# Performance work log

Hardware: AMD Instinct MI355X
Metric: run time of the kernel (lower is better)

## Reference

```python
import jax, jax.numpy as jnp
import numpy as np

E = 1024   # embed_dim
H = 1024   # hidden_dim
NH = 16    # num_heads
HD = H // NH
B, P, C = 2, 1024, 1024


def _layernorm(x, g, b):
    m = jnp.mean(x, axis=-1, keepdims=True)
    v = jnp.mean((x - m) ** 2, axis=-1, keepdims=True)
    return (x - m) / jnp.sqrt(v + 1e-5) * g + b


def _attention(problem, context, Wq, bq, Wk, bk, Wv, bv, mask, num_heads, head_dim, head_out_dim):
    # Faithful to source: head axis LAST in the reshape, mask added AFTER softmax.
    batch = problem.shape[0]
    q = (problem @ Wq + bq).reshape(batch, -1, head_dim, num_heads)      # b i d h
    k = (context @ Wk + bk).reshape(batch, -1, head_dim, num_heads)      # b j d h
    v = (context @ Wv + bv).reshape(batch, -1, head_out_dim, num_heads)  # b j o h
    scores = jnp.einsum('bidh,bjdh->bijh', q, k) / jnp.sqrt(jnp.asarray(head_dim, q.dtype))
    p = jax.nn.softmax(scores, axis=2)
    if mask is not None:
        p = p + mask[..., None]
    out = jnp.einsum('bijh,bjoh->bioh', p, v)
    return out.reshape(batch, -1, head_out_dim * num_heads)


def setup_inputs() -> dict:
    key = jax.random.key(0)
    ks = jax.random.split(key, 20)
    s = 0.02
    inp = {
        'x': jax.random.normal(ks[0], (B, P, E), jnp.float32),
        'context': jax.random.normal(ks[1], (B, C, E), jnp.float32),
        'causal_mask': jnp.zeros((B, P, P), jnp.float32),
        'problem_pad_mask': jnp.zeros((B, P, P), jnp.float32),
        'context_pad_mask': jnp.zeros((B, P, C), jnp.float32),
        # self-attn params (out_dim = E)
        'sa_Wq': jax.random.normal(ks[2], (E, H), jnp.float32) * s, 'sa_bq': jnp.zeros((H,), jnp.float32),
        'sa_Wk': jax.random.normal(ks[3], (E, H), jnp.float32) * s, 'sa_bk': jnp.zeros((H,), jnp.float32),
        'sa_Wv': jax.random.normal(ks[4], (E, E), jnp.float32) * s, 'sa_bv': jnp.zeros((E,), jnp.float32),
        # cross-attn params
        'ca_Wq': jax.random.normal(ks[5], (E, H), jnp.float32) * s, 'ca_bq': jnp.zeros((H,), jnp.float32),
        'ca_Wk': jax.random.normal(ks[6], (E, H), jnp.float32) * s, 'ca_bk': jnp.zeros((H,), jnp.float32),
        'ca_Wv': jax.random.normal(ks[7], (E, E), jnp.float32) * s, 'ca_bv': jnp.zeros((E,), jnp.float32),
        # layernorms
        'ln1_g': jnp.ones((E,), jnp.float32), 'ln1_b': jnp.zeros((E,), jnp.float32),
        'ln2_g': jnp.ones((E,), jnp.float32), 'ln2_b': jnp.zeros((E,), jnp.float32),
        'ln3_g': jnp.ones((E,), jnp.float32), 'ln3_b': jnp.zeros((E,), jnp.float32),
        # mlp
        'mlp_W1': jax.random.normal(ks[8], (E, H), jnp.float32) * s, 'mlp_b1': jnp.zeros((H,), jnp.float32),
        'mlp_W2': jax.random.normal(ks[9], (H, E), jnp.float32) * s, 'mlp_b2': jnp.zeros((E,), jnp.float32),
    }
    return inp


def reference(x, context, causal_mask, problem_pad_mask, context_pad_mask,
              sa_Wq, sa_bq, sa_Wk, sa_bk, sa_Wv, sa_bv,
              ca_Wq, ca_bq, ca_Wk, ca_bk, ca_Wv, ca_bv,
              ln1_g, ln1_b, ln2_g, ln2_b, ln3_g, ln3_b,
              mlp_W1, mlp_b1, mlp_W2, mlp_b2):
    self_attn_mask = causal_mask + problem_pad_mask
    xc = x
    x = _attention(x, x, sa_Wq, sa_bq, sa_Wk, sa_bk, sa_Wv, sa_bv, self_attn_mask, NH, HD, E // NH)
    x = _layernorm(x, ln1_g, ln1_b) + xc
    xc = x
    x = _attention(x, context, ca_Wq, ca_bq, ca_Wk, ca_bk, ca_Wv, ca_bv, context_pad_mask, NH, HD, E // NH)
    x = _layernorm(x, ln2_g, ln2_b) + xc
    xc = x
    x = jax.nn.relu(x @ mlp_W1 + mlp_b1) @ mlp_W2 + mlp_b2
    return _layernorm(x, ln3_g, ln3_b) + xc
```

## Files before the change

kernel.cpp:

```cpp
#include <hip/hip_runtime.h>
#include <math.h>

#define NHEADS 16

typedef __attribute__((ext_vector_type(8))) short bf16x8;
typedef __attribute__((ext_vector_type(4))) float f32x4;

__device__ inline short f2b(float f) {
  unsigned u = __float_as_uint(f);
  u += 0x7fffu + ((u >> 16) & 1u);
  return (short)(u >> 16);
}
__device__ inline float b2f(short s) {
  return __uint_as_float(((unsigned)(unsigned short)s) << 16);
}
__device__ inline void gld16(const void* g, void* l) {
  __builtin_amdgcn_global_load_lds(
      (const __attribute__((address_space(1))) unsigned int*)g,
      (__attribute__((address_space(3))) unsigned int*)l, 16, 0, 0);
}
#define MFMA16(a, b, c) __builtin_amdgcn_mfma_f32_16x16x32_bf16(a, b, c, 0, 0, 0)

__global__ __launch_bounds__(256) void prep_all(
    const float* __restrict__ x, const float* __restrict__ ctx,
    const float* __restrict__ cm, const float* __restrict__ ppm,
    const float* __restrict__ cpm,
    const float* sabq, const float* sabk, const float* sabv,
    const float* cabk, const float* cabv, const float* cabq,
    short* __restrict__ XB, short* __restrict__ CTXB,
    short* __restrict__ MBSA, short* __restrict__ MBCA,
    float* __restrict__ qkvb, float* __restrict__ kvb,
    float* __restrict__ qpb, unsigned* __restrict__ kmaxu) {
  const int blk = blockIdx.x;
  const int t = threadIdx.x;
  const int n4 = 2048 * 1024 / 4;
  if (blk < 8192) {
    int seg = blk >> 11;
    int i = (blk & 2047) * 256 + t;
    if (i >= n4) return;
    float4 va;
    short* out;
    if (seg == 0) { va = ((const float4*)x)[i]; out = XB; }
    else if (seg == 1) { va = ((const float4*)ctx)[i]; out = CTXB; }
    else if (seg == 2) {
      va = ((const float4*)cm)[i];
      float4 vb = ((const float4*)ppm)[i];
      va.x += vb.x; va.y += vb.y; va.z += vb.z; va.w += vb.w;
      out = MBSA;
    } else { va = ((const float4*)cpm)[i]; out = MBCA; }
    short4 s;
    s.x = f2b(va.x); s.y = f2b(va.y); s.z = f2b(va.z); s.w = f2b(va.w);
    ((short4*)out)[i] = s;
  } else {
    if (blk == 8192 && t < 64) kmaxu[t] = 0u;
    int i = (blk - 8192) * 256 + t;
    if (i >= 6144) return;
    int j = i & 1023;
    int pj = ((j & 63) << 4) | (j >> 6);
    int sec = i >> 10;
    if (sec == 0) qkvb[j] = sabq[pj];
    else if (sec == 1) qkvb[1024 + j] = sabk[pj];
    else if (sec == 2) qkvb[2048 + j] = sabv[pj];
    else if (sec == 3) kvb[j] = cabk[pj];
    else if (sec == 4) kvb[1024 + j] = cabv[pj];
    else qpb[j] = cabq[pj];
  }
}

__global__ __launch_bounds__(256) void wtrans(
    const float* W0, const float* W1, const float* W2, const float* W3,
    const float* W4, const float* W5, const float* W6, const float* W7,
    short* __restrict__ out) {
  __shared__ float t[64][65];
  const float* W;
  switch (blockIdx.z) {
    case 0: W = W0; break; case 1: W = W1; break;
    case 2: W = W2; break; case 3: W = W3; break;
    case 4: W = W4; break; case 5: W = W5; break;
    case 6: W = W6; break; default: W = W7; break;
  }
  const int permute = (blockIdx.z < 6) ? 1 : 0;
  short* o = out + (size_t)blockIdx.z * 1024 * 1024;
  const int tid = threadIdx.x;
  const int n0 = blockIdx.x * 64, k0 = blockIdx.y * 64;
  const int cg = (tid & 15) * 4, rg = tid >> 4;
  #pragma unroll
  for (int r = 0; r < 4; ++r) {
    int kl = rg + r * 16;
    float4 v = *(const float4*)(W + (size_t)(k0 + kl) * 1024 + n0 + cg);
    t[kl][cg + 0] = v.x; t[kl][cg + 1] = v.y;
    t[kl][cg + 2] = v.z; t[kl][cg + 3] = v.w;
  }
  __syncthreads();
  #pragma unroll
  for (int r = 0; r < 4; ++r) {
    int nl = rg + r * 16;
    int n = n0 + nl;
    int nrow = permute ? (((n & 15) << 6) | (n >> 4)) : n;
    short4 s;
    s.x = f2b(t[cg + 0][nl]); s.y = f2b(t[cg + 1][nl]);
    s.z = f2b(t[cg + 2][nl]); s.w = f2b(t[cg + 3][nl]);
    *(short4*)(o + (size_t)nrow * 1024 + k0 + cg) = s;
  }
}

__global__ __launch_bounds__(256) void knorm(const short* __restrict__ kh,
                                             unsigned* __restrict__ kmax) {
  const int bh = blockIdx.x, part = blockIdx.y;
  const int tid = threadIdx.x;
  const short* base = kh + (size_t)bh * 65536 +
                      (size_t)(part * 128 + (tid >> 1)) * 64 + (tid & 1) * 32;
  const bf16x8* rp = (const bf16x8*)base;
  float ssq = 0.f;
  #pragma unroll
  for (int c = 0; c < 4; ++c) {
    bf16x8 v = rp[c];
    #pragma unroll
    for (int e = 0; e < 8; ++e) { float f = b2f(v[e]); ssq += f * f; }
  }
  ssq += __shfl_xor(ssq, 1, 64);
  float mx = ssq;
  #pragma unroll
  for (int off = 2; off < 64; off <<= 1) mx = fmaxf(mx, __shfl_xor(mx, off, 64));
  __shared__ float wm[4];
  if ((tid & 63) == 0) wm[tid >> 6] = mx;
  __syncthreads();
  if (tid == 0)
    atomicMax(kmax + bh,
              __float_as_uint(fmaxf(fmaxf(wm[0], wm[1]), fmaxf(wm[2], wm[3]))));
}

template <int TN>
__global__ __launch_bounds__(256) void gemmT(
    const short* __restrict__ A, const short* __restrict__ Bt,
    const float* __restrict__ bias,
    void* __restrict__ C0, short* __restrict__ C1, short* __restrict__ C2,
    int mode, int relu, int ny,
    const short* __restrict__ A2, const short* __restrict__ Bt2,
    const float* __restrict__ bias2,
    void* __restrict__ D0, short* __restrict__ D1, short* __restrict__ D2,
    int mode2, int relu2, int ny2) {
  if (blockIdx.z == 1) {
    A = A2; Bt = Bt2; bias = bias2;
    C0 = D0; C1 = D1; C2 = D2; mode = mode2; relu = relu2; ny = ny2;
  }
  if ((int)blockIdx.y >= ny) return;

  constexpr int NT = TN / 32;
  constexpr int BR = TN / 4;
  __shared__ short As[64 * 64];
  __shared__ short Bs[TN * 64];
  const int tid = threadIdx.x;
  const int w = tid >> 6, l = tid & 63;
  const int ln = l & 15, lq = l >> 4;
  const int wm = w >> 1, wn = w & 1;
  const int m0 = blockIdx.x * 64, n0 = blockIdx.y * TN;
  const int K = 1024;

  f32x4 acc[2][NT];
  #pragma unroll
  for (int s = 0; s < 2; ++s)
    #pragma unroll
    for (int t = 0; t < NT; ++t) acc[s][t] = (f32x4){0.f, 0.f, 0.f, 0.f};

  const int srow = l >> 3;
  const int sch = (l & 7) ^ srow;
  const short* ga = A + (size_t)(m0 + w * 16 + srow) * K + sch * 8;
  const short* gb = Bt + (size_t)(n0 + w * BR + srow) * K + sch * 8;
  short* la = &As[w * 16 * 64];
  short* lb = &Bs[w * BR * 64];

  for (int k0 = 0; k0 < K; k0 += 64) {
    __syncthreads();
    gld16(ga + k0, la);
    gld16(ga + (size_t)8 * K + k0, la + 512);
    #pragma unroll
    for (int rb = 0; rb < BR / 8; ++rb)
      gld16(gb + (size_t)rb * 8 * K + k0, lb + rb * 512);
    __syncthreads();
    #pragma unroll
    for (int kc = 0; kc < 2; ++kc) {
      const int co = ((kc * 4 + lq) ^ (ln & 7)) * 8;
      bf16x8 af[2], bf[NT];
      af[0] = *(const bf16x8*)&As[(wm * 32 + ln) * 64 + co];
      af[1] = *(const bf16x8*)&As[(wm * 32 + 16 + ln) * 64 + co];
      #pragma unroll
      for (int t = 0; t < NT; ++t)
        bf[t] = *(const bf16x8*)&Bs[(wn * (TN / 2) + t * 16 + ln) * 64 + co];
      #pragma unroll
      for (int s = 0; s < 2; ++s)
        #pragma unroll
        for (int t = 0; t < NT; ++t)
          acc[s][t] = MFMA16(af[s], bf[t], acc[s][t]);
    }
  }

  float bv[NT];
  #pragma unroll
  for (int t = 0; t < NT; ++t) bv[t] = bias[n0 + wn * (TN / 2) + t * 16 + ln];

  #pragma unroll
  for (int s = 0; s < 2; ++s) {
    #pragma unroll
    for (int t = 0; t < NT; ++t) {
      #pragma unroll
      for (int r = 0; r < 4; ++r) {
        int m = m0 + wm * 32 + s * 16 + lq * 4 + r;
        int n = n0 + wn * (TN / 2) + t * 16 + ln;
        float v = acc[s][t][r] + bv[t];
        if (relu) v = fmaxf(v, 0.f);
        int bb = m >> 10, ii = m & 1023;
        if (mode == 0) {
          ((float*)C0)[(size_t)m * 1024 + n] = v;
        } else if (mode == 1) {
          ((short*)C0)[(size_t)m * 1024 + n] = f2b(v);
        } else if (mode == 2) {
          int hh = n >> 6, d = n & 63;
          ((short*)C0)[(((size_t)(bb * 16 + hh)) * 1024 + ii) * 64 + d] = f2b(v);
        } else if (mode == 3) {
          int sel = n >> 10, g = n & 1023;
          int hh = g >> 6, d = g & 63;
          if (sel == 0)
            ((short*)C0)[(((size_t)(bb * 16 + hh)) * 1024 + ii) * 64 + d] = f2b(v);
          else if (sel == 1)
            C1[(((size_t)(bb * 16 + hh)) * 1024 + ii) * 64 + d] = f2b(v);
          else
            C2[(((size_t)(bb * 16 + hh)) * 64 + d) * 1024 + ii] = f2b(v);
        } else {
          int sel = n >> 10, g = n & 1023;
          int hh = g >> 6, d = g & 63;
          if (sel == 0)
            C1[(((size_t)(bb * 16 + hh)) * 1024 + ii) * 64 + d] = f2b(v);
          else
            C2[(((size_t)(bb * 16 + hh)) * 64 + d) * 1024 + ii] = f2b(v);
        }
      }
    }
  }
}

__global__ __launch_bounds__(256) void attn_flash(
    const short* __restrict__ qh, const short* __restrict__ kh,
    const short* __restrict__ vt, const short* __restrict__ maskb,
    const unsigned* __restrict__ kmax, float* __restrict__ out) {
  __shared__ short Ks[64 * 64];
  __shared__ short Vs[64 * 64];
  __shared__ short Msk[64 * 64];
  __shared__ short Ps[4][16 * 72];
  __shared__ float Ml[64];
  const int tid = threadIdx.x;
  const int w = tid >> 6, l = tid & 63;
  const int ln = l & 15, lq = l >> 4;
  const int it = blockIdx.x, h = blockIdx.y, b = blockIdx.z;
  const int i0 = it * 64;
  const int bh = b * 16 + h;
  const size_t bho = (size_t)bh * 65536;

  const short* qp = qh + bho + (size_t)(i0 + w * 16 + ln) * 64 + lq * 8;
  bf16x8 qf0 = *(const bf16x8*)qp;
  bf16x8 qf1 = *(const bf16x8*)(qp + 32);

  float ssq = 0.f;
  #pragma unroll
  for (int e = 0; e < 8; ++e) {
    float f0 = b2f(qf0[e]), f1 = b2f(qf1[e]);
    ssq += f0 * f0 + f1 * f1;
  }
  ssq += __shfl_xor(ssq, 16, 64);
  ssq += __shfl_xor(ssq, 32, 64);
  float km = sqrtf(__uint_as_float(kmax[bh])) * 1.0001f;
  if (lq == 0) Ml[w * 16 + ln] = sqrtf(ssq) * km * 0.125f + 1e-3f;
  float Mr[4], lac[4];
  #pragma unroll
  for (int r = 0; r < 4; ++r) { Mr[r] = Ml[w * 16 + lq * 4 + r]; lac[r] = 0.f; }

  const int srow = l >> 3;
  const int sch = (l & 7) ^ (srow & 7);
  const short* gk = kh + bho + (size_t)(w * 16 + srow) * 64 + sch * 8;
  const short* gv = vt + bho + (size_t)(w * 16 + srow) * 1024 + sch * 8;
  const short* gm = maskb + ((size_t)(b * 1024 + i0 + w * 16 + srow)) * 1024 + sch * 8;
  short* lk = &Ks[w * 1024];
  short* lv = &Vs[w * 1024];
  short* lm = &Msk[w * 1024];
  short* PsW = &Ps[w][0];

  f32x4 oa[4], mo[4];
  #pragma unroll
  for (int os = 0; os < 4; ++os) {
    oa[os] = (f32x4){0.f, 0.f, 0.f, 0.f};
    mo[os] = (f32x4){0.f, 0.f, 0.f, 0.f};
  }

  const int c0 = (lq ^ (ln & 7)) * 8;
  const int c1 = ((4 | lq) ^ (ln & 7)) * 8;

  for (int jt = 0; jt < 16; ++jt) {
    __syncthreads();
    gld16(gk + (size_t)jt * 4096, lk);
    gld16(gk + (size_t)jt * 4096 + 512, lk + 512);
    gld16(gv + (size_t)jt * 64, lv);
    gld16(gv + (size_t)jt * 64 + 8192, lv + 512);
    gld16(gm + (size_t)jt * 64, lm);
    gld16(gm + (size_t)jt * 64 + 8192, lm + 512);
    __syncthreads();

    f32x4 sa[4];
    #pragma unroll
    for (int js = 0; js < 4; ++js) {
      const short* kr = &Ks[(js * 16 + ln) * 64];
      bf16x8 kb0 = *(const bf16x8*)(kr + c0);
      bf16x8 kb1 = *(const bf16x8*)(kr + c1);
      f32x4 s = (f32x4){0.f, 0.f, 0.f, 0.f};
      s = MFMA16(qf0, kb0, s);
      s = MFMA16(qf1, kb1, s);
      sa[js] = s;
    }
    #pragma unroll
    for (int js = 0; js < 4; ++js)
      #pragma unroll
      for (int r = 0; r < 4; ++r) {
        float p = __expf(sa[js][r] * 0.125f - Mr[r]);
        lac[r] += p;
        PsW[(lq * 4 + r) * 72 + js * 16 + ln] = f2b(p);
      }
    bf16x8 pa0 = *(const bf16x8*)&PsW[ln * 72 + lq * 8];
    bf16x8 pa1 = *(const bf16x8*)&PsW[ln * 72 + 32 + lq * 8];
    const short* mr = &Msk[(w * 16 + ln) * 64];
    bf16x8 ma0 = *(const bf16x8*)(mr + c0);
    bf16x8 ma1 = *(const bf16x8*)(mr + c1);
    #pragma unroll
    for (int os = 0; os < 4; ++os) {
      const short* vr = &Vs[(os * 16 + ln) * 64];
      bf16x8 vb0 = *(const bf16x8*)(vr + c0);
      bf16x8 vb1 = *(const bf16x8*)(vr + c1);
      oa[os] = MFMA16(pa0, vb0, oa[os]);
      oa[os] = MFMA16(pa1, vb1, oa[os]);
      mo[os] = MFMA16(ma0, vb0, mo[os]);
      mo[os] = MFMA16(ma1, vb1, mo[os]);
    }
  }

  #pragma unroll
  for (int r = 0; r < 4; ++r) {
    lac[r] += __shfl_xor(lac[r], 1, 64);
    lac[r] += __shfl_xor(lac[r], 2, 64);
    lac[r] += __shfl_xor(lac[r], 4, 64);
    lac[r] += __shfl_xor(lac[r], 8, 64);
  }
  float inv[4];
  #pragma unroll
  for (int r = 0; r < 4; ++r) inv[r] = 1.f / lac[r];

  #pragma unroll
  for (int os = 0; os < 4; ++os)
    #pragma unroll
    for (int r = 0; r < 4; ++r) {
      int row = i0 + w * 16 + lq * 4 + r;
      int o = os * 16 + ln;
      out[bho + (size_t)row * 64 + o] = oa[os][r] * inv[r] + mo[os][r];
    }
}

__global__ __launch_bounds__(256) void ln_kernel(
    const float* __restrict__ x, const short* __restrict__ res,
    const float* __restrict__ g, const float* __restrict__ be,
    void* __restrict__ outp, int out_bf16, int inmode) {
  const int row = blockIdx.x;
  const int tid = threadIdx.x;
  float4 v;
  if (inmode == 0) {
    v = ((const float4*)(x + (size_t)row * 1024))[tid];
  } else {
    int b = row >> 10, i = row & 1023;
    const float* base = x + (size_t)b * 16 * 65536 + (size_t)i * 64;
    int o = tid >> 2, h0 = (tid & 3) * 4;
    v.x = base[(size_t)(h0 + 0) * 65536 + o];
    v.y = base[(size_t)(h0 + 1) * 65536 + o];
    v.z = base[(size_t)(h0 + 2) * 65536 + o];
    v.w = base[(size_t)(h0 + 3) * 65536 + o];
  }
  float s = v.x + v.y + v.z + v.w;
  float sq = v.x * v.x + v.y * v.y + v.z * v.z + v.w * v.w;
  #pragma unroll
  for (int off = 32; off > 0; off >>= 1) {
    s += __shfl_down(s, off, 64);
    sq += __shfl_down(sq, off, 64);
  }
  __shared__ float rs[4], rq[4], stat[2];
  int wave = tid >> 6, lane = tid & 63;
  if (lane == 0) { rs[wave] = s; rq[wave] = sq; }
  __syncthreads();
  if (tid == 0) {
    float S = rs[0] + rs[1] + rs[2] + rs[3];
    float Q = rq[0] + rq[1] + rq[2] + rq[3];
    float mean = S * (1.f / 1024.f);
    float var = Q * (1.f / 1024.f) - mean * mean;
    stat[0] = mean;
    stat[1] = rsqrtf(var + 1e-5f);
  }
  __syncthreads();
  float mean = stat[0], rstd = stat[1];
  float4 g4 = ((const float4*)g)[tid];
  float4 b4 = ((const float4*)be)[tid];
  short4 r4 = ((const short4*)(res + (size_t)row * 1024))[tid];
  float o0 = (v.x - mean) * rstd * g4.x + b4.x + b2f(r4.x);
  float o1 = (v.y - mean) * rstd * g4.y + b4.y + b2f(r4.y);
  float o2 = (v.z - mean) * rstd * g4.z + b4.z + b2f(r4.z);
  float o3 = (v.w - mean) * rstd * g4.w + b4.w + b2f(r4.w);
  if (out_bf16) {
    short4 o;
    o.x = f2b(o0); o.y = f2b(o1); o.z = f2b(o2); o.w = f2b(o3);
    ((short4*)outp)[(size_t)row * 256 + tid] = o;
  } else {
    float4 o = {o0, o1, o2, o3};
    ((float4*)outp)[(size_t)row * 256 + tid] = o;
  }
}

extern "C" void kernel_launch(void* const* d_in, const int* in_sizes, int n_in,
                              void* d_out, int out_size, void* d_ws, size_t ws_size,
                              hipStream_t stream) {
  const float* x    = (const float*)d_in[0];
  const float* ctx  = (const float*)d_in[1];
  const float* cm   = (const float*)d_in[2];
  const float* ppm  = (const float*)d_in[3];
  const float* cpm  = (const float*)d_in[4];
  const float* saWq = (const float*)d_in[5];
  const float* sabq = (const float*)d_in[6];
  const float* saWk = (const float*)d_in[7];
  const float* sabk = (const float*)d_in[8];
  const float* saWv = (const float*)d_in[9];
  const float* sabv = (const float*)d_in[10];
  const float* caWq = (const float*)d_in[11];
  const float* cabq = (const float*)d_in[12];
  const float* caWk = (const float*)d_in[13];
  const float* cabk = (const float*)d_in[14];
  const float* caWv = (const float*)d_in[15];
  const float* cabv = (const float*)d_in[16];
  const float* ln1g = (const float*)d_in[17];
  const float* ln1b = (const float*)d_in[18];
  const float* ln2g = (const float*)d_in[19];
  const float* ln2b = (const float*)d_in[20];
  const float* ln3g = (const float*)d_in[21];
  const float* ln3b = (const float*)d_in[22];
  const float* W1   = (const float*)d_in[23];
  const float* b1   = (const float*)d_in[24];
  const float* W2   = (const float*)d_in[25];
  const float* b2   = (const float*)d_in[26];

  char* ws = (char*)d_ws;
  const size_t MB = 1024 * 1024;
  short* WT       = (short*)(ws);
  float* qkvb     = (float*)(ws + 16 * MB);
  float* kvb      = (float*)(ws + 16 * MB + 16384);
  float* qpb      = (float*)(ws + 16 * MB + 32768);
  unsigned* kmaxu = (unsigned*)(ws + 16 * MB + 49152);
  short* MBSA  = (short*)(ws + 17 * MB);
  short* MBCA  = (short*)(ws + 21 * MB);
  short* XB    = (short*)(ws + 25 * MB);
  short* CTXB  = (short*)(ws + 29 * MB);
  short* QH    = (short*)(ws + 33 * MB);
  short* KH    = (short*)(ws + 37 * MB);
  short* VT    = (short*)(ws + 41 * MB);
  float* S3    = (float*)(ws + 45 * MB);
  short* X1B   = (short*)(ws + 53 * MB);
  short* X2B   = MBSA;
  short* HB    = CTXB;
  float* outp  = (float*)d_out;

  dim3 lg(2048);
  const short* dsp = nullptr;
  const float* dfp = nullptr;

  wtrans<<<dim3(16, 16, 8), 256, 0, stream>>>(saWq, saWk, saWv, caWk, caWv,
                                              caWq, W1, W2, WT);
  prep_all<<<dim3(8216), 256, 0, stream>>>(x, ctx, cm, ppm, cpm,
                                           sabq, sabk, sabv, cabk, cabv, cabq,
                                           XB, CTXB, MBSA, MBCA, qkvb, kvb, qpb,
                                           kmaxu);

  gemmT<128><<<dim3(32, 24, 1), 256, 0, stream>>>(
      XB, WT, qkvb, QH, KH, VT, 3, 0, 24,
      dsp, dsp, dfp, nullptr, nullptr, nullptr, 0, 0, 0);
  knorm<<<dim3(32, 8), 256, 0, stream>>>(KH, kmaxu);
  attn_flash<<<dim3(16, 16, 2), 256, 0, stream>>>(QH, KH, VT, MBSA, kmaxu, S3);
  ln_kernel<<<lg, 256, 0, stream>>>(S3, XB, ln1g, ln1b, X1B, 1, 1);

  gemmT<128><<<dim3(32, 16, 2), 256, 0, stream>>>(
      X1B, WT + 5 * 1048576, qpb, QH, nullptr, nullptr, 2, 0, 8,
      CTXB, WT + 3 * 1048576, kvb, nullptr, KH, VT, 4, 0, 16);
  knorm<<<dim3(32, 8), 256, 0, stream>>>(KH, kmaxu + 32);
  attn_flash<<<dim3(16, 16, 2), 256, 0, stream>>>(QH, KH, VT, MBCA, kmaxu + 32, S3);
  ln_kernel<<<lg, 256, 0, stream>>>(S3, X1B, ln2g, ln2b, X2B, 1, 1);

  gemmT<64><<<dim3(32, 16, 1), 256, 0, stream>>>(
      X2B, WT + 6 * 1048576, b1, HB, nullptr, nullptr, 1, 1, 16,
      dsp, dsp, dfp, nullptr, nullptr, nullptr, 0, 0, 0);
  gemmT<64><<<dim3(32, 16, 1), 256, 0, stream>>>(
      HB, WT + 7 * 1048576, b2, S3, nullptr, nullptr, 0, 0, 16,
      dsp, dsp, dfp, nullptr, nullptr, nullptr, 0, 0, 0);
  ln_kernel<<<lg, 256, 0, stream>>>(S3, X2B, ln3g, ln3b, outp, 0, 0);
}
```

Before: 299.0 us.

## Fuse prep kernels, fold key-norm into GEMM epilogue, widen attention K tiles

Merges the weight transpose into the prep kernel, so one launch does the fp32-to-bf16 conversion, the bias permutation and the weight transpose. The separate key-norm kernels are removed. Each GEMM block now computes per-row squared norms of its K tile in the epilogue and publishes the maximum with atomicMax. The cross-attention K/V projection moves into the first GEMM launch (z=2) with separate buffers, so it runs alongside the self-attention QKV projection. The attention kernel loads 128-key tiles per iteration, halving the barriers and loop trips, and the softmax upper-bound margin is loosened. The changes add LDS use and epilogue shuffles in exchange for fewer launches and less serialisation.

```diff
diff --git a/kernel.cpp b/kernel.cpp
--- a/kernel.cpp
+++ b/kernel.cpp
@@ -21,22 +21,26 @@
 }
 #define MFMA16(a, b, c) __builtin_amdgcn_mfma_f32_16x16x32_bf16(a, b, c, 0, 0, 0)
 
-__global__ __launch_bounds__(256) void prep_all(
+__global__ __launch_bounds__(256) void prep_wt(
     const float* __restrict__ x, const float* __restrict__ ctx,
     const float* __restrict__ cm, const float* __restrict__ ppm,
     const float* __restrict__ cpm,
     const float* sabq, const float* sabk, const float* sabv,
     const float* cabk, const float* cabv, const float* cabq,
+    const float* W0, const float* W1, const float* W2, const float* W3,
+    const float* W4, const float* W5, const float* W6, const float* W7,
     short* __restrict__ XB, short* __restrict__ CTXB,
     short* __restrict__ MBSA, short* __restrict__ MBCA,
     float* __restrict__ qkvb, float* __restrict__ kvb,
-    float* __restrict__ qpb, unsigned* __restrict__ kmaxu) {
+    float* __restrict__ qpb, unsigned* __restrict__ kmaxu,
+    short* __restrict__ WT) {
+  __shared__ float t[64][65];
   const int blk = blockIdx.x;
-  const int t = threadIdx.x;
+  const int tid = threadIdx.x;
   const int n4 = 2048 * 1024 / 4;
   if (blk < 8192) {
     int seg = blk >> 11;
-    int i = (blk & 2047) * 256 + t;
+    int i = (blk & 2047) * 256 + tid;
     if (i >= n4) return;
     float4 va;
     short* out;
@@ -51,9 +55,11 @@
     short4 s;
     s.x = f2b(va.x); s.y = f2b(va.y); s.z = f2b(va.z); s.w = f2b(va.w);
     ((short4*)out)[i] = s;
-  } else {
-    if (blk == 8192 && t < 64) kmaxu[t] = 0u;
-    int i = (blk - 8192) * 256 + t;
+    return;
+  }
+  if (blk < 8216) {
+    if (blk == 8192 && tid < 64) kmaxu[tid] = 0u;
+    int i = (blk - 8192) * 256 + tid;
     if (i >= 6144) return;
     int j = i & 1023;
     int pj = ((j & 63) << 4) | (j >> 6);
@@ -64,25 +70,21 @@
     else if (sec == 3) kvb[j] = cabk[pj];
     else if (sec == 4) kvb[1024 + j] = cabv[pj];
     else qpb[j] = cabq[pj];
-  }
-}
-
-__global__ __launch_bounds__(256) void wtrans(
-    const float* W0, const float* W1, const float* W2, const float* W3,
-    const float* W4, const float* W5, const float* W6, const float* W7,
-    short* __restrict__ out) {
-  __shared__ float t[64][65];
+    return;
+  }
+  const int blk2 = blk - 8216;
+  const int wz = blk2 >> 8;
+  const int rem = blk2 & 255;
   const float* W;
-  switch (blockIdx.z) {
+  switch (wz) {
     case 0: W = W0; break; case 1: W = W1; break;
     case 2: W = W2; break; case 3: W = W3; break;
     case 4: W = W4; break; case 5: W = W5; break;
     case 6: W = W6; break; default: W = W7; break;
   }
-  const int permute = (blockIdx.z < 6) ? 1 : 0;
-  short* o = out + (size_t)blockIdx.z * 1024 * 1024;
-  const int tid = threadIdx.x;
-  const int n0 = blockIdx.x * 64, k0 = blockIdx.y * 64;
+  const int permute = (wz < 6) ? 1 : 0;
+  short* o = WT + (size_t)wz * 1024 * 1024;
+  const int n0 = (rem & 15) * 64, k0 = (rem >> 4) * 64;
   const int cg = (tid & 15) * 4, rg = tid >> 4;
   #pragma unroll
   for (int r = 0; r < 4; ++r) {
@@ -102,32 +104,6 @@
     s.z = f2b(t[cg + 2][nl]); s.w = f2b(t[cg + 3][nl]);
     *(short4*)(o + (size_t)nrow * 1024 + k0 + cg) = s;
   }
-}
-
-__global__ __launch_bounds__(256) void knorm(const short* __restrict__ kh,
-                                             unsigned* __restrict__ kmax) {
-  const int bh = blockIdx.x, part = blockIdx.y;
-  const int tid = threadIdx.x;
-  const short* base = kh + (size_t)bh * 65536 +
-                      (size_t)(part * 128 + (tid >> 1)) * 64 + (tid & 1) * 32;
-  const bf16x8* rp = (const bf16x8*)base;
-  float ssq = 0.f;
-  #pragma unroll
-  for (int c = 0; c < 4; ++c) {
-    bf16x8 v = rp[c];
-    #pragma unroll
-    for (int e = 0; e < 8; ++e) { float f = b2f(v[e]); ssq += f * f; }
-  }
-  ssq += __shfl_xor(ssq, 1, 64);
-  float mx = ssq;
-  #pragma unroll
-  for (int off = 2; off < 64; off <<= 1) mx = fmaxf(mx, __shfl_xor(mx, off, 64));
-  __shared__ float wm[4];
-  if ((tid & 63) == 0) wm[tid >> 6] = mx;
-  __syncthreads();
-  if (tid == 0)
-    atomicMax(kmax + bh,
-              __float_as_uint(fmaxf(fmaxf(wm[0], wm[1]), fmaxf(wm[2], wm[3]))));
 }
 
 template <int TN>
@@ -139,7 +115,8 @@
     const short* __restrict__ A2, const short* __restrict__ Bt2,
     const float* __restrict__ bias2,
     void* __restrict__ D0, short* __restrict__ D1, short* __restrict__ D2,
-    int mode2, int relu2, int ny2) {
+    int mode2, int relu2, int ny2,
+    unsigned* __restrict__ kout) {
   if (blockIdx.z == 1) {
     A = A2; Bt = Bt2; bias = bias2;
     C0 = D0; C1 = D1; C2 = D2; mode = mode2; relu = relu2; ny = ny2;
@@ -237,23 +214,54 @@
       }
     }
   }
+
+  if constexpr (TN == 128) {
+    const int nb = n0 + wn * 64;
+    const int selw = nb >> 10;
+    if ((mode == 3 && selw == 1) || (mode == 4 && selw == 0)) {
+      const int slotbase = (mode == 3) ? 0 : 32;
+      const int bb = m0 >> 10;
+      const int hh = (nb & 1023) >> 6;
+      float mx = 0.f;
+      #pragma unroll
+      for (int s = 0; s < 2; ++s)
+        #pragma unroll
+        for (int r = 0; r < 4; ++r) {
+          float ss = 0.f;
+          #pragma unroll
+          for (int t = 0; t < 4; ++t) {
+            float v = acc[s][t][r] + bv[t];
+            ss += v * v;
+          }
+          ss += __shfl_xor(ss, 1, 64);
+          ss += __shfl_xor(ss, 2, 64);
+          ss += __shfl_xor(ss, 4, 64);
+          ss += __shfl_xor(ss, 8, 64);
+          mx = fmaxf(mx, ss);
+        }
+      mx = fmaxf(mx, __shfl_xor(mx, 16, 64));
+      mx = fmaxf(mx, __shfl_xor(mx, 32, 64));
+      if (l == 0)
+        atomicMax(kout + slotbase + bb * 16 + hh, __float_as_uint(mx));
+    }
+  }
 }
 
 __global__ __launch_bounds__(256) void attn_flash(
     const short* __restrict__ qh, const short* __restrict__ kh,
     const short* __restrict__ vt, const short* __restrict__ maskb,
     const unsigned* __restrict__ kmax, float* __restrict__ out) {
-  __shared__ short Ks[64 * 64];
-  __shared__ short Vs[64 * 64];
-  __shared__ short Msk[64 * 64];
+  __shared__ short Ks[128 * 64];
+  __shared__ short Vs[64 * 128];
+  __shared__ short Msk[64 * 128];
   __shared__ short Ps[4][16 * 72];
   __shared__ float Ml[64];
   const int tid = threadIdx.x;
   const int w = tid >> 6, l = tid & 63;
   const int ln = l & 15, lq = l >> 4;
-  const int it = blockIdx.x, h = blockIdx.y, b = blockIdx.z;
-  const int i0 = it * 64;
-  const int bh = b * 16 + h;
+  const int i0 = blockIdx.x * 64;
+  const int b = blockIdx.z;
+  const int bh = b * 16 + blockIdx.y;
   const size_t bho = (size_t)bh * 65536;
 
   const short* qp = qh + bho + (size_t)(i0 + w * 16 + ln) * 64 + lq * 8;
@@ -268,20 +276,22 @@
   }
   ssq += __shfl_xor(ssq, 16, 64);
   ssq += __shfl_xor(ssq, 32, 64);
-  float km = sqrtf(__uint_as_float(kmax[bh])) * 1.0001f;
+  float km = sqrtf(__uint_as_float(kmax[bh])) * 1.005f;
   if (lq == 0) Ml[w * 16 + ln] = sqrtf(ssq) * km * 0.125f + 1e-3f;
   float Mr[4], lac[4];
   #pragma unroll
   for (int r = 0; r < 4; ++r) { Mr[r] = Ml[w * 16 + lq * 4 + r]; lac[r] = 0.f; }
 
-  const int srow = l >> 3;
-  const int sch = (l & 7) ^ (srow & 7);
-  const short* gk = kh + bho + (size_t)(w * 16 + srow) * 64 + sch * 8;
-  const short* gv = vt + bho + (size_t)(w * 16 + srow) * 1024 + sch * 8;
-  const short* gm = maskb + ((size_t)(b * 1024 + i0 + w * 16 + srow)) * 1024 + sch * 8;
-  short* lk = &Ks[w * 1024];
-  short* lv = &Vs[w * 1024];
-  short* lm = &Msk[w * 1024];
+  const int r8 = l >> 3;
+  const int c8 = (l & 7) ^ r8;
+  const int r4 = l >> 4;
+  const int cva = (l & 15) ^ r4;
+  const short* gkb = kh + bho + (size_t)(w * 32 + r8) * 64 + c8 * 8;
+  const short* gvb = vt + bho + (size_t)(w * 16 + r4) * 1024;
+  const short* gmb = maskb + ((size_t)(b * 1024 + i0 + w * 16 + r4)) * 1024;
+  short* lkb = &Ks[w * 32 * 64];
+  short* lvb = &Vs[w * 16 * 128];
+  short* lmb = &Msk[w * 16 * 128];
   short* PsW = &Ps[w][0];
 
   f32x4 oa[4], mo[4];
@@ -294,49 +304,56 @@
   const int c0 = (lq ^ (ln & 7)) * 8;
   const int c1 = ((4 | lq) ^ (ln & 7)) * 8;
 
-  for (int jt = 0; jt < 16; ++jt) {
+  for (int jt = 0; jt < 8; ++jt) {
+    const int j0 = jt * 128;
     __syncthreads();
-    gld16(gk + (size_t)jt * 4096, lk);
-    gld16(gk + (size_t)jt * 4096 + 512, lk + 512);
-    gld16(gv + (size_t)jt * 64, lv);
-    gld16(gv + (size_t)jt * 64 + 8192, lv + 512);
-    gld16(gm + (size_t)jt * 64, lm);
-    gld16(gm + (size_t)jt * 64 + 8192, lm + 512);
+    #pragma unroll
+    for (int gi = 0; gi < 4; ++gi)
+      gld16(gkb + (size_t)(j0 + gi * 8) * 64, lkb + gi * 512);
+    #pragma unroll
+    for (int gi = 0; gi < 4; ++gi) {
+      int cc = (cva ^ ((gi & 1) << 2)) * 8;
+      gld16(gvb + (size_t)gi * 4096 + j0 + cc, lvb + gi * 512);
+      gld16(gmb + (size_t)gi * 4096 + j0 + cc, lmb + gi * 512);
+    }
     __syncthreads();
 
-    f32x4 sa[4];
-    #pragma unroll
-    for (int js = 0; js < 4; ++js) {
-      const short* kr = &Ks[(js * 16 + ln) * 64];
-      bf16x8 kb0 = *(const bf16x8*)(kr + c0);
-      bf16x8 kb1 = *(const bf16x8*)(kr + c1);
-      f32x4 s = (f32x4){0.f, 0.f, 0.f, 0.f};
-      s = MFMA16(qf0, kb0, s);
-      s = MFMA16(qf1, kb1, s);
-      sa[js] = s;
-    }
-    #pragma unroll
-    for (int js = 0; js < 4; ++js)
-      #pragma unroll
-      for (int r = 0; r < 4; ++r) {
-        float p = __expf(sa[js][r] * 0.125f - Mr[r]);
-        lac[r] += p;
-        PsW[(lq * 4 + r) * 72 + js * 16 + ln] = f2b(p);
+    #pragma unroll
+    for (int jh = 0; jh < 2; ++jh) {
+      f32x4 sa[4];
+      #pragma unroll
+      for (int js = 0; js < 4; ++js) {
+        const short* kr = &Ks[(jh * 64 + js * 16 + ln) * 64];
+        bf16x8 kb0 = *(const bf16x8*)(kr + c0);
+        bf16x8 kb1 = *(const bf16x8*)(kr + c1);
+        f32x4 s = (f32x4){0.f, 0.f, 0.f, 0.f};
+        s = MFMA16(qf0, kb0, s);
+        s = MFMA16(qf1, kb1, s);
+        sa[js] = s;
       }
-    bf16x8 pa0 = *(const bf16x8*)&PsW[ln * 72 + lq * 8];
-    bf16x8 pa1 = *(const bf16x8*)&PsW[ln * 72 + 32 + lq * 8];
-    const short* mr = &Msk[(w * 16 + ln) * 64];
-    bf16x8 ma0 = *(const bf16x8*)(mr + c0);
-    bf16x8 ma1 = *(const bf16x8*)(mr + c1);
-    #pragma unroll
-    for (int os = 0; os < 4; ++os) {
-      const short* vr = &Vs[(os * 16 + ln) * 64];
-      bf16x8 vb0 = *(const bf16x8*)(vr + c0);
-      bf16x8 vb1 = *(const bf16x8*)(vr + c1);
-      oa[os] = MFMA16(pa0, vb0, oa[os]);
-      oa[os] = MFMA16(pa1, vb1, oa[os]);
-      mo[os] = MFMA16(ma0, vb0, mo[os]);
-      mo[os] = MFMA16(ma1, vb1, mo[os]);
+      #pragma unroll
+      for (int js = 0; js < 4; ++js)
+        #pragma unroll
+        for (int r = 0; r < 4; ++r) {
+          float p = __expf(sa[js][r] * 0.125f - Mr[r]);
+          lac[r] += p;
+          PsW[(lq * 4 + r) * 72 + js * 16 + ln] = f2b(p);
+        }
+      bf16x8 pa0 = *(const bf16x8*)&PsW[ln * 72 + lq * 8];
+      bf16x8 pa1 = *(const bf16x8*)&PsW[ln * 72 + 32 + lq * 8];
+      const short* mr2 = &Msk[(w * 16 + ln) * 128 + jh * 64];
+      bf16x8 ma0 = *(const bf16x8*)(mr2 + c0);
+      bf16x8 ma1 = *(const bf16x8*)(mr2 + c1);
+      #pragma unroll
+      for (int os = 0; os < 4; ++os) {
+        const short* vr = &Vs[(os * 16 + ln) * 128 + jh * 64];
+        bf16x8 vb0 = *(const bf16x8*)(vr + c0);
+        bf16x8 vb1 = *(const bf16x8*)(vr + c1);
+        oa[os] = MFMA16(pa0, vb0, oa[os]);
+        oa[os] = MFMA16(pa1, vb1, oa[os]);
+        mo[os] = MFMA16(ma0, vb0, mo[os]);
+        mo[os] = MFMA16(ma1, vb1, mo[os]);
+      }
     }
   }
 
@@ -464,6 +481,8 @@
   short* VT    = (short*)(ws + 41 * MB);
   float* S3    = (float*)(ws + 45 * MB);
   short* X1B   = (short*)(ws + 53 * MB);
+  short* KH2   = (short*)(ws + 57 * MB);
+  short* VT2   = (short*)(ws + 61 * MB);
   short* X2B   = MBSA;
   short* HB    = CTXB;
   float* outp  = (float*)d_out;
@@ -472,32 +491,31 @@
   const short* dsp = nullptr;
   const float* dfp = nullptr;
 
-  wtrans<<<dim3(16, 16, 8), 256, 0, stream>>>(saWq, saWk, saWv, caWk, caWv,
-                                              caWq, W1, W2, WT);
-  prep_all<<<dim3(8216), 256, 0, stream>>>(x, ctx, cm, ppm, cpm,
-                                           sabq, sabk, sabv, cabk, cabv, cabq,
-                                           XB, CTXB, MBSA, MBCA, qkvb, kvb, qpb,
-                                           kmaxu);
-
-  gemmT<128><<<dim3(32, 24, 1), 256, 0, stream>>>(
+  prep_wt<<<dim3(10264), 256, 0, stream>>>(
+      x, ctx, cm, ppm, cpm, sabq, sabk, sabv, cabk, cabv, cabq,
+      saWq, saWk, saWv, caWk, caWv, caWq, W1, W2,
+      XB, CTXB, MBSA, MBCA, qkvb, kvb, qpb, kmaxu, WT);
+
+  gemmT<128><<<dim3(32, 24, 2), 256, 0, stream>>>(
       XB, WT, qkvb, QH, KH, VT, 3, 0, 24,
-      dsp, dsp, dfp, nullptr, nullptr, nullptr, 0, 0, 0);
-  knorm<<<dim3(32, 8), 256, 0, stream>>>(KH, kmaxu);
+      CTXB, WT + 3 * 1048576, kvb, nullptr, KH2, VT2, 4, 0, 16, kmaxu);
+
   attn_flash<<<dim3(16, 16, 2), 256, 0, stream>>>(QH, KH, VT, MBSA, kmaxu, S3);
   ln_kernel<<<lg, 256, 0, stream>>>(S3, XB, ln1g, ln1b, X1B, 1, 1);
 
-  gemmT<128><<<dim3(32, 16, 2), 256, 0, stream>>>(
-      X1B, WT + 5 * 1048576, qpb, QH, nullptr, nullptr, 2, 0, 8,
-      CTXB, WT + 3 * 1048576, kvb, nullptr, KH, VT, 4, 0, 16);
-  knorm<<<dim3(32, 8), 256, 0, stream>>>(KH, kmaxu + 32);
-  attn_flash<<<dim3(16, 16, 2), 256, 0, stream>>>(QH, KH, VT, MBCA, kmaxu + 32, S3);
+  gemmT<64><<<dim3(32, 16, 1), 256, 0, stream>>>(
+      X1B, WT + 5 * 1048576, qpb, QH, nullptr, nullptr, 2, 0, 16,
+      dsp, dsp, dfp, nullptr, nullptr, nullptr, 0, 0, 0, kmaxu);
+
+  attn_flash<<<dim3(16, 16, 2), 256, 0, stream>>>(QH, KH2, VT2, MBCA,
+                                                  kmaxu + 32, S3);
   ln_kernel<<<lg, 256, 0, stream>>>(S3, X1B, ln2g, ln2b, X2B, 1, 1);
 
   gemmT<64><<<dim3(32, 16, 1), 256, 0, stream>>>(
       X2B, WT + 6 * 1048576, b1, HB, nullptr, nullptr, 1, 1, 16,
-      dsp, dsp, dfp, nullptr, nullptr, nullptr, 0, 0, 0);
+      dsp, dsp, dfp, nullptr, nullptr, nullptr, 0, 0, 0, kmaxu);
   gemmT<64><<<dim3(32, 16, 1), 256, 0, stream>>>(
       HB, WT + 7 * 1048576, b2, S3, nullptr, nullptr, 0, 0, 16,
-      dsp, dsp, dfp, nullptr, nullptr, nullptr, 0, 0, 0);
+      dsp, dsp, dfp, nullptr, nullptr, nullptr, 0, 0, 0, kmaxu);
   ln_kernel<<<lg, 256, 0, stream>>>(S3, X2B, ln3g, ln3b, outp, 0, 0);
 }
```

New measurement: 309.7 us. +3.6%, slower.
